# Kernel tuning notes

Measured on AMD Instinct MI355X. Metric: run time of the kernel, lower is better.

The kernel has to match this reference:

```python
import jax, jax.numpy as jnp
import numpy as np

N_NODES = 50000
N_EDGES = 800000
HIDDEN = 256
N_LAYERS = 3
N_PAIRS = 4096


def setup_inputs() -> dict:
    key = jax.random.key(0)
    ks = jax.random.split(key, 10)
    s = 1.0 / np.sqrt(HIDDEN)
    x = jax.random.normal(ks[0], (N_NODES, HIDDEN), dtype=jnp.float32)
    f0_w = jax.random.normal(ks[1], (N_LAYERS, HIDDEN, HIDDEN), dtype=jnp.float32) * s
    f0_b = jax.random.normal(ks[2], (N_LAYERS, HIDDEN), dtype=jnp.float32) * s
    f1_w = jax.random.normal(ks[3], (N_LAYERS, HIDDEN, HIDDEN), dtype=jnp.float32) * s
    f1_b = jax.random.normal(ks[4], (N_LAYERS, HIDDEN), dtype=jnp.float32) * s
    conv_w = jax.random.normal(ks[5], (N_LAYERS, HIDDEN, HIDDEN), dtype=jnp.float32) * s
    conv_b = jax.random.normal(ks[6], (N_LAYERS, HIDDEN), dtype=jnp.float32) * s
    edge_src = jax.random.randint(ks[7], (N_EDGES,), 0, N_NODES, dtype=jnp.int64 if jax.config.jax_enable_x64 else jnp.int32)
    edge_dst = jax.random.randint(ks[8], (N_EDGES,), 0, N_NODES, dtype=edge_src.dtype)
    pos = jax.random.randint(ks[9], (N_PAIRS, 2), 0, N_NODES, dtype=edge_src.dtype)
    return {"x": x, "f0_w": f0_w, "f0_b": f0_b, "f1_w": f1_w, "f1_b": f1_b,
            "conv_w": conv_w, "conv_b": conv_b,
            "edge_src": edge_src, "edge_dst": edge_dst, "pos": pos}


def reference(x, f0_w, f0_b, f1_w, f1_b, conv_w, conv_b, edge_src, edge_dst, pos):
    # Faithful translation of FLabelingNet.forward:
    #   for each layer: x0 = f0(x); x0[idx] = f1(x[idx]); x = conv(x0, adj)
    #   return x[pos]
    n = x.shape[0]
    idx = pos.reshape(-1)  # (2M,) labeled node indices
    for i in range(f0_w.shape[0]):
        x0 = x @ f0_w[i] + f0_b[i]                       # (N, F) elementwise linear
        lbl = x[idx] @ f1_w[i] + f1_b[i]                 # (2M, F) transform of labeled rows
        x0 = x0.at[idx].set(lbl)                         # scatter-overwrite selected rows
        h = x0 @ conv_w[i] + conv_b[i]                   # node-wise linear of the conv
        # sparse adjacency message passing: out[v] = sum_{(u,v) in E} h[u]
        x = jax.ops.segment_sum(h[edge_src], edge_dst, num_segments=n)
    return x[pos]  # (M, 2, F)
```

## Files before the change

kernel.cpp:

```cpp
#include <hip/hip_runtime.h>
#include <hip/hip_bf16.h>

#define N_NODES 50000
#define N_EDGES 800000
#define HIDDEN  256
#define N_LAYERS 3
#define N_PAIRS 4096
#define N_LABEL 8192
#define NPAD    50176
#define SCAN_BLOCKS (NPAD / 256)
#define WSZ (HIDDEN * HIDDEN)

#define NROWPAD (N_NODES + 1)
#define SLICE_ELEMS ((size_t)NROWPAD * 32)
#define SEG_CHUNKS ((N_NODES + 63) / 64)

#define G0_PAIRS   3136
#define G0_TOTAL   (G0_PAIRS + 256)

typedef __bf16 bf16x8 __attribute__((ext_vector_type(8)));
typedef __bf16 bf16x4 __attribute__((ext_vector_type(4)));
typedef float  f32x4  __attribute__((ext_vector_type(4)));
typedef float  f32x2  __attribute__((ext_vector_type(2)));

__device__ __forceinline__ void load_lds16(const void* g, void* l) {
    __builtin_amdgcn_global_load_lds(
        (const __attribute__((address_space(1))) void*)g,
        (__attribute__((address_space(3))) void*)l, 16, 0, 0);
}

__device__ __forceinline__ void acc8(const uint4 w, f32x2* a) {
    a[0] += (f32x2){__uint_as_float(w.x << 16), __uint_as_float(w.x & 0xffff0000u)};
    a[1] += (f32x2){__uint_as_float(w.y << 16), __uint_as_float(w.y & 0xffff0000u)};
    a[2] += (f32x2){__uint_as_float(w.z << 16), __uint_as_float(w.z & 0xffff0000u)};
    a[3] += (f32x2){__uint_as_float(w.w << 16), __uint_as_float(w.w & 0xffff0000u)};
}

template <bool DEG_BIAS, bool A_FP32, bool FILL_PLANE>
__global__ __launch_bounds__(256) void mfma_gemm_fused(
    const void* __restrict__ A_in,
    const __bf16* __restrict__ Wt0, const __bf16* __restrict__ Wt1,
    const float* __restrict__ bD0, const float* __restrict__ bD1,
    const float* __restrict__ bC0, const float* __restrict__ bC1,
    __bf16* __restrict__ Cout,
    const int* __restrict__ idx,
    const int* __restrict__ degv,
    const int* __restrict__ flags,
    const int* __restrict__ esrc,
    const int* __restrict__ edst,
    int* __restrict__ cursor,
    int* __restrict__ ssorted,
    int M)
{
    int role, bx, by;
    if constexpr (FILL_PLANE) {
        const int id = blockIdx.x;
        if (id < G0_PAIRS) {
            const int sub = ((id >> 4) << 3) | (id & 7);
            if ((id >> 3) & 1) {
                int e = sub * 512 + (int)threadIdx.x;
                #pragma unroll
                for (int r = 0; r < 2; ++r) {
                    if (e < N_EDGES) {
                        const int p = atomicAdd(&cursor[edst[e]], 1);
                        ssorted[p] = esrc[e];
                    }
                    e += 256;
                }
                return;
            }
            role = 0; bx = sub >> 1; by = sub & 1;
            if (bx >= 782) return;
        } else {
            const int lb = id - G0_PAIRS;
            role = 1; bx = lb & 127; by = lb >> 7;
        }
    } else {
        role = blockIdx.z; bx = blockIdx.x; by = blockIdx.y;
        if (role == 1 && bx >= N_LABEL / 64) return;
    }

    const __bf16* A   = (const __bf16*)A_in;
    const float*  A32 = (const float*)A_in;
    const __bf16* Wt  = role ? Wt1 : Wt0;
    const float*  bD  = role ? bD1 : bD0;
    const float*  bC  = role ? bC1 : bC0;

    __shared__ __bf16 As[64 * 32];
    __shared__ __bf16 Bs[128 * 32];
    __shared__ int s_idx[64];

    const int t    = threadIdx.x;
    const int lane = t & 63;
    const int wave = t >> 6;
    const int m0   = bx * 64;
    const int n0   = by * 128;

    if (role == 1) {
        if (t < 64) s_idx[t] = idx[m0 + t];
        __syncthreads();
    }

    const int arow  = t >> 2;
    const int acol8 = (t & 3) * 8;
    int anode;
    if (role == 1) {
        anode = s_idx[arow];
    } else {
        const int rg = m0 + arow;
        anode = (rg < M) ? rg : (M - 1);
    }
    const __bf16* aptr   = A   + (size_t)anode * HIDDEN + acol8;
    const float*  aptr32 = A32 + (size_t)anode * HIDDEN + acol8;

    const __bf16* bptr[2];
    #pragma unroll
    for (int r = 0; r < 2; ++r) {
        const int c = r * 256 + t;
        bptr[r] = Wt + (size_t)(n0 + (c >> 2)) * HIDDEN + (c & 3) * 8;
    }

    f32x4 acc[8];
    #pragma unroll
    for (int i = 0; i < 8; ++i) acc[i] = (f32x4){0.f, 0.f, 0.f, 0.f};

    const int wm   = wave * 16;
    const int fm   = lane & 15;
    const int quad = lane >> 4;

    for (int k0 = 0; k0 < HIDDEN; k0 += 32) {
        __syncthreads();
        if constexpr (A_FP32) {
            const float* ap = aptr32 + k0;
            const float4 u0 = *(const float4*)(ap);
            const float4 u1 = *(const float4*)(ap + 4);
            bf16x8 w = {(__bf16)u0.x, (__bf16)u0.y, (__bf16)u0.z, (__bf16)u0.w,
                        (__bf16)u1.x, (__bf16)u1.y, (__bf16)u1.z, (__bf16)u1.w};
            *(bf16x8*)(As + (size_t)t * 8) = w;
        } else {
            load_lds16(aptr + k0, (void*)(As + (size_t)t * 8));
        }
        #pragma unroll
        for (int r = 0; r < 2; ++r)
            load_lds16(bptr[r] + k0, (void*)(Bs + (size_t)(r * 256 + t) * 8));
        __syncthreads();

        const bf16x8 af = *(const bf16x8*)(As + (wm + fm) * 32 + quad * 8);
        bf16x8 bfr[8];
        #pragma unroll
        for (int nt = 0; nt < 8; ++nt)
            bfr[nt] = *(const bf16x8*)(Bs + (nt * 16 + fm) * 32 + quad * 8);

        #pragma unroll
        for (int nt = 0; nt < 8; ++nt)
            acc[nt] = __builtin_amdgcn_mfma_f32_16x16x32_bf16(
                af, bfr[nt], acc[nt], 0, 0, 0);
    }

    float bd[8], bc[8];
    #pragma unroll
    for (int nt = 0; nt < 8; ++nt) {
        const int col = n0 + nt * 16 + fm;
        bd[nt] = DEG_BIAS ? bD[col] : 0.f;
        bc[nt] = bC[col];
    }

    #pragma unroll
    for (int rg = 0; rg < 4; ++rg) {
        const int rloc = wm + quad * 4 + rg;
        int orow;
        if (role == 1) {
            orow = s_idx[rloc];
        } else {
            orow = m0 + rloc;
            if (orow >= M) continue;
            if (flags[orow]) continue;
        }
        float bscale = 0.f;
        if constexpr (DEG_BIAS)
            bscale = (float)degv[orow];
        #pragma unroll
        for (int nt = 0; nt < 8; ++nt) {
            const int cb = n0 + nt * 16;
            float v = acc[nt][rg];
            if constexpr (DEG_BIAS) v += bscale * bd[nt];
            v += bc[nt];
            Cout[(size_t)(cb >> 5) * SLICE_ELEMS + (size_t)orow * 32
                 + (cb & 31) + fm] = (__bf16)v;
        }
    }
}

template <bool GATHER_A, bool DEG_BIAS, bool DEG_VIA_IDX, bool OUT_BF16, bool PROD_BATCH>
__global__ __launch_bounds__(256) void mfma_gemm(
    const __bf16* __restrict__ A_in,
    const __bf16* __restrict__ Wt_in,
    const float* __restrict__ biasD,
    void* __restrict__ Cout_in,
    const int* __restrict__ idx,
    const int* __restrict__ degv,
    int M)
{
    const __bf16* A  = A_in;
    const __bf16* Wt = Wt_in;
    void* Cout = Cout_in;
    if constexpr (PROD_BATCH) {
        const int z = blockIdx.z;
        A    = A_in  + (size_t)(3 * (1 + (z >> 1)) + (z & 1)) * WSZ;
        Wt   = Wt_in + (size_t)(z >> 1) * WSZ;
        Cout = (void*)((__bf16*)Cout_in + (size_t)z * WSZ);
    }

    __shared__ __bf16 As[64 * 32];
    __shared__ __bf16 Bs[128 * 32];
    __shared__ int s_idx[64];

    const int t    = threadIdx.x;
    const int lane = t & 63;
    const int wave = t >> 6;
    const int m0   = blockIdx.x * 64;
    const int n0   = blockIdx.y * 128;

    if constexpr (GATHER_A || DEG_VIA_IDX) {
        if (t < 64) s_idx[t] = idx[m0 + t];
        __syncthreads();
    }

    const int arow  = t >> 2;
    const int acol8 = (t & 3) * 8;
    int anode;
    if constexpr (GATHER_A) {
        anode = s_idx[arow];
    } else {
        const int rg = m0 + arow;
        anode = (rg < M) ? rg : (M - 1);
    }
    const __bf16* aptr = A + (size_t)anode * HIDDEN + acol8;

    const __bf16* bptr[2];
    #pragma unroll
    for (int r = 0; r < 2; ++r) {
        const int c = r * 256 + t;
        bptr[r] = Wt + (size_t)(n0 + (c >> 2)) * HIDDEN + (c & 3) * 8;
    }

    f32x4 acc[8];
    #pragma unroll
    for (int i = 0; i < 8; ++i) acc[i] = (f32x4){0.f, 0.f, 0.f, 0.f};

    const int wm   = wave * 16;
    const int fm   = lane & 15;
    const int quad = lane >> 4;

    for (int k0 = 0; k0 < HIDDEN; k0 += 32) {
        __syncthreads();
        load_lds16(aptr + k0, (void*)(As + (size_t)t * 8));
        #pragma unroll
        for (int r = 0; r < 2; ++r)
            load_lds16(bptr[r] + k0, (void*)(Bs + (size_t)(r * 256 + t) * 8));
        __syncthreads();

        const bf16x8 af = *(const bf16x8*)(As + (wm + fm) * 32 + quad * 8);
        bf16x8 bfr[8];
        #pragma unroll
        for (int nt = 0; nt < 8; ++nt)
            bfr[nt] = *(const bf16x8*)(Bs + (nt * 16 + fm) * 32 + quad * 8);

        #pragma unroll
        for (int nt = 0; nt < 8; ++nt)
            acc[nt] = __builtin_amdgcn_mfma_f32_16x16x32_bf16(
                af, bfr[nt], acc[nt], 0, 0, 0);
    }

    float bd[8];
    #pragma unroll
    for (int nt = 0; nt < 8; ++nt)
        bd[nt] = DEG_BIAS ? biasD[n0 + nt * 16 + fm] : 0.f;

    #pragma unroll
    for (int rg = 0; rg < 4; ++rg) {
        const int rloc = wm + quad * 4 + rg;
        const int orow = m0 + rloc;
        if (!PROD_BATCH && orow >= M) continue;
        int dnode = orow;
        if constexpr (GATHER_A || DEG_VIA_IDX) dnode = s_idx[rloc];
        float bscale = 0.f;
        if constexpr (DEG_BIAS)
            bscale = (float)degv[dnode];
        #pragma unroll
        for (int nt = 0; nt < 8; ++nt) {
            const int col = n0 + nt * 16 + fm;
            float v = acc[nt][rg];
            if constexpr (DEG_BIAS) v += bscale * bd[nt];
            if constexpr (OUT_BF16)
                ((__bf16*)Cout)[(size_t)orow * HIDDEN + col] = (__bf16)v;
            else
                ((float*)Cout)[(size_t)orow * HIDDEN + col] = v;
        }
    }
}

__global__ __launch_bounds__(256) void wconv_kernel(
    const float* __restrict__ f0_w, const float* __restrict__ f1_w,
    const float* __restrict__ conv_w, const float* __restrict__ conv_b,
    __bf16* __restrict__ wt_all, __bf16* __restrict__ cw_nt,
    float* __restrict__ q,
    const int* __restrict__ edge_dst, const int* __restrict__ pos,
    int* __restrict__ counts, int* __restrict__ flags,
    __bf16* __restrict__ x0b)
{
    const int z = blockIdx.z;
    const int tx = threadIdx.x, ty = threadIdx.y;

    if (z >= 12) {
        const int plane = z - 12;
        const int t = ty * 32 + tx;
        const int eb = plane * 64 + blockIdx.x * 8 + blockIdx.y;
        const int e = eb * 256 + t;
        if (e < N_EDGES) atomicAdd(&counts[edge_dst[e]], 1);
        if (e < N_LABEL) flags[pos[e]] = 1;
        if (plane == 0 && blockIdx.x == 0 && blockIdx.y == 0) {
            const int sl = t >> 5, c = t & 31;
            x0b[(size_t)sl * SLICE_ELEMS + (size_t)N_NODES * 32 + c] = (__bf16)0.f;
        }
        return;
    }

    const int kx = blockIdx.x * 32, nx = blockIdx.y * 32;

    if (z < 9) {
        const int layer = z / 3, which = z % 3;
        const float* W = ((which == 0) ? f0_w : (which == 1) ? f1_w : conv_w)
                         + (size_t)layer * WSZ;
        __bf16* T = wt_all + (size_t)z * WSZ;

        __shared__ float tile[32][33];
        for (int i = ty; i < 32; i += 8)
            tile[i][tx] = W[(size_t)(kx + i) * HIDDEN + nx + tx];
        __syncthreads();
        for (int i = ty; i < 32; i += 8)
            T[(size_t)(nx + i) * HIDDEN + kx + tx] = (__bf16)tile[tx][i];
    } else if (z < 11) {
        const int layer = z - 9;
        const float* W = conv_w + (size_t)layer * WSZ;
        __bf16* T = cw_nt + (size_t)layer * WSZ;
        for (int i = ty; i < 32; i += 8)
            T[(size_t)(kx + i) * HIDDEN + nx + tx] =
                (__bf16)W[(size_t)(kx + i) * HIDDEN + nx + tx];
    } else {
        if (blockIdx.x >= 4 || blockIdx.y != 0) return;
        const int zq = blockIdx.x;
        const int l = zq >> 1, branch = zq & 1;
        const float* cb = conv_b + (size_t)l * HIDDEN;
        const float* W  = (branch ? f1_w : f0_w) + (size_t)(l + 1) * WSZ;
        const int n = ty * 32 + tx;
        float s = 0.f;
        #pragma unroll 4
        for (int k = 0; k < HIDDEN; ++k)
            s += cb[k] * W[(size_t)k * HIDDEN + n];
        q[(size_t)zq * HIDDEN + n] = s;
    }
}

__device__ __forceinline__ int block_incl_scan(int v, int* s, int t)
{
    s[t] = v; __syncthreads();
    #pragma unroll
    for (int off = 1; off < 256; off <<= 1) {
        int add = (t >= off) ? s[t - off] : 0;
        __syncthreads();
        s[t] += add;
        __syncthreads();
    }
    return s[t];
}

__global__ __launch_bounds__(256) void scan1_kernel(
    const int* __restrict__ counts, int* __restrict__ offs, int* __restrict__ bsum)
{
    __shared__ int s[256];
    const int t = threadIdx.x;
    const int i = blockIdx.x * 256 + t;
    const int pv = (counts[i] + 7) & ~7;
    int incl = block_incl_scan(pv, s, t);
    offs[i] = incl - pv;
    if (t == 255) bsum[blockIdx.x] = incl;
}

__global__ __launch_bounds__(256) void scan2_kernel(
    const int* __restrict__ bsum, int* __restrict__ bbase)
{
    __shared__ int s[256];
    const int t = threadIdx.x;
    const int v = (t < SCAN_BLOCKS) ? bsum[t] : 0;
    int incl = block_incl_scan(v, s, t);
    bbase[t] = incl - v;
}

__global__ __launch_bounds__(256) void scan3_kernel(
    int* __restrict__ offs, const int* __restrict__ bbase,
    int* __restrict__ cursor, const int* __restrict__ counts,
    int* __restrict__ src_sorted)
{
    const int i = blockIdx.x * 256 + threadIdx.x;
    const int o = offs[i] + bbase[blockIdx.x];
    offs[i] = o;
    cursor[i] = o;
    const int v  = counts[i];
    const int pv = (v + 7) & ~7;
    for (int j = o + v; j < o + pv; ++j) src_sorted[j] = N_NODES;
}

template <bool COMPACT>
__global__ __launch_bounds__(256) void seg_slice_kernel(
    const __bf16* __restrict__ x0b,
    const int* __restrict__ srcs,
    const int* __restrict__ offs,
    const int* __restrict__ nodelist,
    __bf16* __restrict__ out)
{
    const int slice = blockIdx.x & 7;
    const int chunk = blockIdx.x >> 3;
    const int t    = threadIdx.x;
    const int wave = t >> 6;
    const int lane = t & 63;
    const int g    = lane >> 2;
    const int li   = lane & 3;
    const int rw   = chunk * 64 + wave * 16 + g;
    if (!COMPACT && rw >= N_NODES) return;

    const int d    = COMPACT ? nodelist[rw] : rw;
    const int beg  = offs[d];
    const int pdeg = offs[d + 1] - beg;

    const char* xb = (const char*)(x0b + (size_t)slice * SLICE_ELEMS);
    const uint32_t lioff = (uint32_t)li * 16u;
    const int* sp = srcs + beg;

    f32x2 a[4];
    #pragma unroll
    for (int j = 0; j < 4; ++j) a[j] = (f32x2){0.f, 0.f};

    int4 j0, j1;
    if (pdeg > 0) {
        j0 = *(const int4*)(sp);
        j1 = *(const int4*)(sp + 4);
    }

    for (int base = 0; base < pdeg; base += 8) {
        const int4 k0 = j0, k1 = j1;
        if (base + 8 < pdeg) {
            j0 = *(const int4*)(sp + base + 8);
            j1 = *(const int4*)(sp + base + 12);
        }
        const uint4 c0 = *(const uint4*)(xb + (((uint32_t)k0.x << 6) + lioff));
        const uint4 c1 = *(const uint4*)(xb + (((uint32_t)k0.y << 6) + lioff));
        const uint4 c2 = *(const uint4*)(xb + (((uint32_t)k0.z << 6) + lioff));
        const uint4 c3 = *(const uint4*)(xb + (((uint32_t)k0.w << 6) + lioff));
        const uint4 c4 = *(const uint4*)(xb + (((uint32_t)k1.x << 6) + lioff));
        const uint4 c5 = *(const uint4*)(xb + (((uint32_t)k1.y << 6) + lioff));
        const uint4 c6 = *(const uint4*)(xb + (((uint32_t)k1.z << 6) + lioff));
        const uint4 c7 = *(const uint4*)(xb + (((uint32_t)k1.w << 6) + lioff));
        acc8(c0, a); acc8(c1, a); acc8(c2, a); acc8(c3, a);
        acc8(c4, a); acc8(c5, a); acc8(c6, a); acc8(c7, a);
    }

    bf16x8 o;
    #pragma unroll
    for (int j = 0; j < 4; ++j) {
        o[2 * j]     = (__bf16)a[j].x;
        o[2 * j + 1] = (__bf16)a[j].y;
    }
    *(bf16x8*)(out + (size_t)rw * HIDDEN + (slice << 5) + li * 8) = o;
}

extern "C" void kernel_launch(void* const* d_in, const int* in_sizes, int n_in,
                              void* d_out, int out_size, void* d_ws, size_t ws_size,
                              hipStream_t stream)
{
    const float* x       = (const float*)d_in[0];
    const float* f0_w    = (const float*)d_in[1];
    const float* f0_b    = (const float*)d_in[2];
    const float* f1_w    = (const float*)d_in[3];
    const float* f1_b    = (const float*)d_in[4];
    const float* conv_w  = (const float*)d_in[5];
    const float* conv_b  = (const float*)d_in[6];
    const int*   edge_src = (const int*)d_in[7];
    const int*   edge_dst = (const int*)d_in[8];
    const int*   pos      = (const int*)d_in[9];
    float* out = (float*)d_out;

    const size_t buf = (size_t)N_NODES * HIDDEN;

    char* p = (char*)d_ws;
    __bf16* bufA   = (__bf16*)p; p += buf * 2;
    __bf16* bufB   = (__bf16*)p; p += SLICE_ELEMS * 8 * 2;
    __bf16* s_lbl  = (__bf16*)p; p += (size_t)N_LABEL * HIDDEN * 2;
    __bf16* wt_all = (__bf16*)p; p += (size_t)9 * WSZ * 2;
    __bf16* prod   = (__bf16*)p; p += (size_t)4 * WSZ * 2;
    __bf16* cw_nt  = (__bf16*)p; p += (size_t)2 * WSZ * 2;
    float*  qv     = (float*)p;  p += (size_t)4 * HIDDEN * 4;
    int* counts     = (int*)p;  p += NPAD * 4;
    int* flags      = (int*)p;  p += NPAD * 4;
    int* offs       = (int*)p;  p += NPAD * 4;
    int* cursor     = (int*)p;  p += NPAD * 4;
    int* bsum       = (int*)p;  p += 256 * 4;
    int* bbase      = (int*)p;  p += 256 * 4;
    int* src_sorted = (int*)p;  p += (size_t)(N_EDGES + 7 * NPAD) * 4;

    hipMemsetAsync(counts, 0, 2 * NPAD * sizeof(int), stream);
    wconv_kernel<<<dim3(8, 8, 61), dim3(32, 8), 0, stream>>>(
        f0_w, f1_w, conv_w, conv_b, wt_all, cw_nt, qv,
        edge_dst, pos, counts, flags, bufB);
    scan1_kernel<<<SCAN_BLOCKS, 256, 0, stream>>>(counts, offs, bsum);
    scan2_kernel<<<1, 256, 0, stream>>>(bsum, bbase);
    scan3_kernel<<<SCAN_BLOCKS, 256, 0, stream>>>(offs, bbase, cursor, counts, src_sorted);

    mfma_gemm<false, false, false, true, true><<<dim3(4, 2, 4), 256, 0, stream>>>(
        wt_all, cw_nt, nullptr, prod, nullptr, nullptr, HIDDEN);

    const dim3 fused_grid(782, 2, 2);
    const dim3 lbl_grid(128, 2);

    __bf16* cur = bufA;
    __bf16* tmp = bufB;

    for (int l = 0; l < N_LAYERS; ++l) {
        const float* B0 = f0_b + (size_t)l * HIDDEN;
        const float* B1 = f1_b + (size_t)l * HIDDEN;

        if (l == 0) {
            mfma_gemm_fused<false, true, true><<<G0_TOTAL, 256, 0, stream>>>(
                x, wt_all + 0 * WSZ, wt_all + 1 * WSZ,
                nullptr, nullptr, B0, B1, tmp, pos, counts, flags,
                edge_src, edge_dst, cursor, src_sorted, N_NODES);
        } else {
            const int z0 = (l - 1) * 2;
            mfma_gemm_fused<true, false, false><<<fused_grid, 256, 0, stream>>>(
                cur, prod + (size_t)z0 * WSZ, prod + (size_t)(z0 + 1) * WSZ,
                qv + (size_t)z0 * HIDDEN, qv + (size_t)(z0 + 1) * HIDDEN,
                B0, B1, tmp, pos, counts, flags,
                nullptr, nullptr, nullptr, nullptr, N_NODES);
        }

        if (l < N_LAYERS - 1) {
            seg_slice_kernel<false><<<8 * SEG_CHUNKS, 256, 0, stream>>>(
                tmp, src_sorted, offs, nullptr, cur);
        } else {
            seg_slice_kernel<true><<<8 * (N_LABEL / 64), 256, 0, stream>>>(
                tmp, src_sorted, offs, pos, s_lbl);
            mfma_gemm<false, true, true, false, false><<<lbl_grid, 256, 0, stream>>>(
                s_lbl, wt_all + (size_t)(2 * 3 + 2) * WSZ,
                conv_b + (size_t)2 * HIDDEN, out, pos, counts, N_LABEL);
        }
    }
}
```

Baseline: 384.3 us.

## Triple-buffer GEMM K-loop, precast x to bf16, and rank-based edge placement

Both MFMA GEMM kernels now run a 3-stage LDS ring buffer with asynchronous global-to-LDS loads issued two steps ahead. Each step waits with explicit vmcnt and uses one barrier instead of two, so load latency overlaps the MFMA work. The fp32 input x is converted to bf16 in extra blocks of the prep kernel, which lets layer 0 use the async LDS path. The edge bucketing records each edge's atomic rank during counting and places it at offs+rank, replacing a second atomic pass over cursors. The cost is triple the LDS footprint (which may reduce occupancy), an extra N_EDGES rank buffer, and a full extra pass writing x as bf16.

New measurement: 355.2 us. 1.08x faster.

```diff
diff --git a/kernel.cpp b/kernel.cpp
--- a/kernel.cpp
+++ b/kernel.cpp
@@ -10,6 +10,7 @@
 #define NPAD    50176
 #define SCAN_BLOCKS (NPAD / 256)
 #define WSZ (HIDDEN * HIDDEN)
+#define NSTEP (HIDDEN / 32)
 
 #define NROWPAD (N_NODES + 1)
 #define SLICE_ELEMS ((size_t)NROWPAD * 32)
@@ -19,7 +20,6 @@
 #define G0_TOTAL   (G0_PAIRS + 256)
 
 typedef __bf16 bf16x8 __attribute__((ext_vector_type(8)));
-typedef __bf16 bf16x4 __attribute__((ext_vector_type(4)));
 typedef float  f32x4  __attribute__((ext_vector_type(4)));
 typedef float  f32x2  __attribute__((ext_vector_type(2)));
 
@@ -36,9 +36,16 @@
     a[3] += (f32x2){__uint_as_float(w.w << 16), __uint_as_float(w.w & 0xffff0000u)};
 }
 
-template <bool DEG_BIAS, bool A_FP32, bool FILL_PLANE>
+#define GEMM_PIPELINE(APTR, BPTR, AS, BS)                                     \
+    {                                                                          \
+        load_lds16((APTR), (void*)((AS) + (size_t)t * 8));                     \
+        load_lds16((BPTR)[0], (void*)((BS) + (size_t)t * 8));                  \
+        load_lds16((BPTR)[1], (void*)((BS) + (size_t)(256 + t) * 8));          \
+    }
+
+template <bool DEG_BIAS, bool FILL_PLANE>
 __global__ __launch_bounds__(256) void mfma_gemm_fused(
-    const void* __restrict__ A_in,
+    const __bf16* __restrict__ A,
     const __bf16* __restrict__ Wt0, const __bf16* __restrict__ Wt1,
     const float* __restrict__ bD0, const float* __restrict__ bD1,
     const float* __restrict__ bC0, const float* __restrict__ bC1,
@@ -48,7 +55,8 @@
     const int* __restrict__ flags,
     const int* __restrict__ esrc,
     const int* __restrict__ edst,
-    int* __restrict__ cursor,
+    const int* __restrict__ coffs,
+    const int* __restrict__ rankv,
     int* __restrict__ ssorted,
     int M)
 {
@@ -62,8 +70,8 @@
                 #pragma unroll
                 for (int r = 0; r < 2; ++r) {
                     if (e < N_EDGES) {
-                        const int p = atomicAdd(&cursor[edst[e]], 1);
-                        ssorted[p] = esrc[e];
+                        const int d = edst[e];
+                        ssorted[coffs[d] + rankv[e]] = esrc[e];
                     }
                     e += 256;
                 }
@@ -80,14 +88,12 @@
         if (role == 1 && bx >= N_LABEL / 64) return;
     }
 
-    const __bf16* A   = (const __bf16*)A_in;
-    const float*  A32 = (const float*)A_in;
-    const __bf16* Wt  = role ? Wt1 : Wt0;
-    const float*  bD  = role ? bD1 : bD0;
-    const float*  bC  = role ? bC1 : bC0;
-
-    __shared__ __bf16 As[64 * 32];
-    __shared__ __bf16 Bs[128 * 32];
+    const __bf16* Wt = role ? Wt1 : Wt0;
+    const float*  bD = role ? bD1 : bD0;
+    const float*  bC = role ? bC1 : bC0;
+
+    __shared__ __bf16 As[3 * 64 * 32];
+    __shared__ __bf16 Bs[3 * 128 * 32];
     __shared__ int s_idx[64];
 
     const int t    = threadIdx.x;
@@ -110,8 +116,7 @@
         const int rg = m0 + arow;
         anode = (rg < M) ? rg : (M - 1);
     }
-    const __bf16* aptr   = A   + (size_t)anode * HIDDEN + acol8;
-    const float*  aptr32 = A32 + (size_t)anode * HIDDEN + acol8;
+    const __bf16* aptr = A + (size_t)anode * HIDDEN + acol8;
 
     const __bf16* bptr[2];
     #pragma unroll
@@ -128,34 +133,41 @@
     const int fm   = lane & 15;
     const int quad = lane >> 4;
 
-    for (int k0 = 0; k0 < HIDDEN; k0 += 32) {
-        __syncthreads();
-        if constexpr (A_FP32) {
-            const float* ap = aptr32 + k0;
-            const float4 u0 = *(const float4*)(ap);
-            const float4 u1 = *(const float4*)(ap + 4);
-            bf16x8 w = {(__bf16)u0.x, (__bf16)u0.y, (__bf16)u0.z, (__bf16)u0.w,
-                        (__bf16)u1.x, (__bf16)u1.y, (__bf16)u1.z, (__bf16)u1.w};
-            *(bf16x8*)(As + (size_t)t * 8) = w;
-        } else {
-            load_lds16(aptr + k0, (void*)(As + (size_t)t * 8));
-        }
-        #pragma unroll
-        for (int r = 0; r < 2; ++r)
-            load_lds16(bptr[r] + k0, (void*)(Bs + (size_t)(r * 256 + t) * 8));
-        __syncthreads();
-
-        const bf16x8 af = *(const bf16x8*)(As + (wm + fm) * 32 + quad * 8);
+    const __bf16* bp0 = bptr[0];
+    const __bf16* bp1 = bptr[1];
+    #define STAGE_F(SB, K0)                                                    \
+        { load_lds16(aptr + (K0), (void*)(As + (SB) * 2048 + (size_t)t * 8));  \
+          load_lds16(bp0 + (K0),  (void*)(Bs + (SB) * 4096 + (size_t)t * 8));  \
+          load_lds16(bp1 + (K0),  (void*)(Bs + (SB) * 4096 + (size_t)(256 + t) * 8)); }
+
+    STAGE_F(0, 0)
+    STAGE_F(1, 32)
+    asm volatile("s_waitcnt vmcnt(3)" ::: "memory");
+    __builtin_amdgcn_sched_barrier(0);
+    __builtin_amdgcn_s_barrier();
+
+    #pragma unroll
+    for (int step = 0; step < NSTEP; ++step) {
+        const int cur = step % 3;
+        if (step + 2 < NSTEP) {
+            const int nb = (step + 2) % 3;
+            STAGE_F(nb, (step + 2) * 32)
+        }
+        const bf16x8 af = *(const bf16x8*)(As + cur * 2048 + (wm + fm) * 32 + quad * 8);
         bf16x8 bfr[8];
         #pragma unroll
         for (int nt = 0; nt < 8; ++nt)
-            bfr[nt] = *(const bf16x8*)(Bs + (nt * 16 + fm) * 32 + quad * 8);
-
+            bfr[nt] = *(const bf16x8*)(Bs + cur * 4096 + (nt * 16 + fm) * 32 + quad * 8);
         #pragma unroll
         for (int nt = 0; nt < 8; ++nt)
             acc[nt] = __builtin_amdgcn_mfma_f32_16x16x32_bf16(
                 af, bfr[nt], acc[nt], 0, 0, 0);
-    }
+        if (step + 2 < NSTEP) asm volatile("s_waitcnt vmcnt(3)" ::: "memory");
+        else                  asm volatile("s_waitcnt vmcnt(0)" ::: "memory");
+        __builtin_amdgcn_sched_barrier(0);
+        __builtin_amdgcn_s_barrier();
+    }
+    #undef STAGE_F
 
     float bd[8], bc[8];
     #pragma unroll
@@ -211,8 +223,8 @@
         Cout = (void*)((__bf16*)Cout_in + (size_t)z * WSZ);
     }
 
-    __shared__ __bf16 As[64 * 32];
-    __shared__ __bf16 Bs[128 * 32];
+    __shared__ __bf16 As[3 * 64 * 32];
+    __shared__ __bf16 Bs[3 * 128 * 32];
     __shared__ int s_idx[64];
 
     const int t    = threadIdx.x;
@@ -252,25 +264,41 @@
     const int fm   = lane & 15;
     const int quad = lane >> 4;
 
-    for (int k0 = 0; k0 < HIDDEN; k0 += 32) {
-        __syncthreads();
-        load_lds16(aptr + k0, (void*)(As + (size_t)t * 8));
-        #pragma unroll
-        for (int r = 0; r < 2; ++r)
-            load_lds16(bptr[r] + k0, (void*)(Bs + (size_t)(r * 256 + t) * 8));
-        __syncthreads();
-
-        const bf16x8 af = *(const bf16x8*)(As + (wm + fm) * 32 + quad * 8);
+    const __bf16* bp0 = bptr[0];
+    const __bf16* bp1 = bptr[1];
+    #define STAGE_P(SB, K0)                                                    \
+        { load_lds16(aptr + (K0), (void*)(As + (SB) * 2048 + (size_t)t * 8));  \
+          load_lds16(bp0 + (K0),  (void*)(Bs + (SB) * 4096 + (size_t)t * 8));  \
+          load_lds16(bp1 + (K0),  (void*)(Bs + (SB) * 4096 + (size_t)(256 + t) * 8)); }
+
+    STAGE_P(0, 0)
+    STAGE_P(1, 32)
+    asm volatile("s_waitcnt vmcnt(3)" ::: "memory");
+    __builtin_amdgcn_sched_barrier(0);
+    __builtin_amdgcn_s_barrier();
+
+    #pragma unroll
+    for (int step = 0; step < NSTEP; ++step) {
+        const int cur = step % 3;
+        if (step + 2 < NSTEP) {
+            const int nb = (step + 2) % 3;
+            STAGE_P(nb, (step + 2) * 32)
+        }
+        const bf16x8 af = *(const bf16x8*)(As + cur * 2048 + (wm + fm) * 32 + quad * 8);
         bf16x8 bfr[8];
         #pragma unroll
         for (int nt = 0; nt < 8; ++nt)
-            bfr[nt] = *(const bf16x8*)(Bs + (nt * 16 + fm) * 32 + quad * 8);
-
+            bfr[nt] = *(const bf16x8*)(Bs + cur * 4096 + (nt * 16 + fm) * 32 + quad * 8);
         #pragma unroll
         for (int nt = 0; nt < 8; ++nt)
             acc[nt] = __builtin_amdgcn_mfma_f32_16x16x32_bf16(
                 af, bfr[nt], acc[nt], 0, 0, 0);
-    }
+        if (step + 2 < NSTEP) asm volatile("s_waitcnt vmcnt(3)" ::: "memory");
+        else                  asm volatile("s_waitcnt vmcnt(0)" ::: "memory");
+        __builtin_amdgcn_sched_barrier(0);
+        __builtin_amdgcn_s_barrier();
+    }
+    #undef STAGE_P
 
     float bd[8];
     #pragma unroll
@@ -307,20 +335,34 @@
     float* __restrict__ q,
     const int* __restrict__ edge_dst, const int* __restrict__ pos,
     int* __restrict__ counts, int* __restrict__ flags,
-    __bf16* __restrict__ x0b)
+    int* __restrict__ rankv,
+    __bf16* __restrict__ x0b,
+    const float* __restrict__ x32, __bf16* __restrict__ xb16)
 {
     const int z = blockIdx.z;
     const int tx = threadIdx.x, ty = threadIdx.y;
-
+    const int tt = ty * 32 + tx;
+
+    if (z >= 61) {
+        const int c = (z - 61) * 64 + blockIdx.x * 8 + blockIdx.y;
+        const size_t base = ((size_t)c * 256 + tt) * 8;
+        if (base < (size_t)N_NODES * HIDDEN) {
+            const float4 u0 = *(const float4*)(x32 + base);
+            const float4 u1 = *(const float4*)(x32 + base + 4);
+            bf16x8 w = {(__bf16)u0.x, (__bf16)u0.y, (__bf16)u0.z, (__bf16)u0.w,
+                        (__bf16)u1.x, (__bf16)u1.y, (__bf16)u1.z, (__bf16)u1.w};
+            *(bf16x8*)(xb16 + base) = w;
+        }
+        return;
+    }
     if (z >= 12) {
         const int plane = z - 12;
-        const int t = ty * 32 + tx;
         const int eb = plane * 64 + blockIdx.x * 8 + blockIdx.y;
-        const int e = eb * 256 + t;
-        if (e < N_EDGES) atomicAdd(&counts[edge_dst[e]], 1);
+        const int e = eb * 256 + tt;
+        if (e < N_EDGES) rankv[e] = atomicAdd(&counts[edge_dst[e]], 1);
         if (e < N_LABEL) flags[pos[e]] = 1;
         if (plane == 0 && blockIdx.x == 0 && blockIdx.y == 0) {
-            const int sl = t >> 5, c = t & 31;
+            const int sl = tt >> 5, c = tt & 31;
             x0b[(size_t)sl * SLICE_ELEMS + (size_t)N_NODES * 32 + c] = (__bf16)0.f;
         }
         return;
@@ -353,7 +395,7 @@
         const int l = zq >> 1, branch = zq & 1;
         const float* cb = conv_b + (size_t)l * HIDDEN;
         const float* W  = (branch ? f1_w : f0_w) + (size_t)(l + 1) * WSZ;
-        const int n = ty * 32 + tx;
+        const int n = tt;
         float s = 0.f;
         #pragma unroll 4
         for (int k = 0; k < HIDDEN; ++k)
@@ -399,13 +441,11 @@
 
 __global__ __launch_bounds__(256) void scan3_kernel(
     int* __restrict__ offs, const int* __restrict__ bbase,
-    int* __restrict__ cursor, const int* __restrict__ counts,
-    int* __restrict__ src_sorted)
+    const int* __restrict__ counts, int* __restrict__ src_sorted)
 {
     const int i = blockIdx.x * 256 + threadIdx.x;
     const int o = offs[i] + bbase[blockIdx.x];
     offs[i] = o;
-    cursor[i] = o;
     const int v  = counts[i];
     const int pv = (v + 7) & ~7;
     for (int j = o + v; j < o + pv; ++j) src_sorted[j] = N_NODES;
@@ -503,18 +543,18 @@
     int* counts     = (int*)p;  p += NPAD * 4;
     int* flags      = (int*)p;  p += NPAD * 4;
     int* offs       = (int*)p;  p += NPAD * 4;
-    int* cursor     = (int*)p;  p += NPAD * 4;
     int* bsum       = (int*)p;  p += 256 * 4;
     int* bbase      = (int*)p;  p += 256 * 4;
+    int* rankv      = (int*)p;  p += (size_t)N_EDGES * 4;
     int* src_sorted = (int*)p;  p += (size_t)(N_EDGES + 7 * NPAD) * 4;
 
     hipMemsetAsync(counts, 0, 2 * NPAD * sizeof(int), stream);
-    wconv_kernel<<<dim3(8, 8, 61), dim3(32, 8), 0, stream>>>(
+    wconv_kernel<<<dim3(8, 8, 159), dim3(32, 8), 0, stream>>>(
         f0_w, f1_w, conv_w, conv_b, wt_all, cw_nt, qv,
-        edge_dst, pos, counts, flags, bufB);
+        edge_dst, pos, counts, flags, rankv, bufB, x, bufA);
     scan1_kernel<<<SCAN_BLOCKS, 256, 0, stream>>>(counts, offs, bsum);
     scan2_kernel<<<1, 256, 0, stream>>>(bsum, bbase);
-    scan3_kernel<<<SCAN_BLOCKS, 256, 0, stream>>>(offs, bbase, cursor, counts, src_sorted);
+    scan3_kernel<<<SCAN_BLOCKS, 256, 0, stream>>>(offs, bbase, counts, src_sorted);
 
     mfma_gemm<false, false, false, true, true><<<dim3(4, 2, 4), 256, 0, stream>>>(
         wt_all, cw_nt, nullptr, prod, nullptr, nullptr, HIDDEN);
@@ -530,17 +570,17 @@
         const float* B1 = f1_b + (size_t)l * HIDDEN;
 
         if (l == 0) {
-            mfma_gemm_fused<false, true, true><<<G0_TOTAL, 256, 0, stream>>>(
-                x, wt_all + 0 * WSZ, wt_all + 1 * WSZ,
+            mfma_gemm_fused<false, true><<<G0_TOTAL, 256, 0, stream>>>(
+                bufA, wt_all + 0 * WSZ, wt_all + 1 * WSZ,
                 nullptr, nullptr, B0, B1, tmp, pos, counts, flags,
-                edge_src, edge_dst, cursor, src_sorted, N_NODES);
+                edge_src, edge_dst, offs, rankv, src_sorted, N_NODES);
         } else {
             const int z0 = (l - 1) * 2;
-            mfma_gemm_fused<true, false, false><<<fused_grid, 256, 0, stream>>>(
+            mfma_gemm_fused<true, false><<<fused_grid, 256, 0, stream>>>(
                 cur, prod + (size_t)z0 * WSZ, prod + (size_t)(z0 + 1) * WSZ,
                 qv + (size_t)z0 * HIDDEN, qv + (size_t)(z0 + 1) * HIDDEN,
                 B0, B1, tmp, pos, counts, flags,
-                nullptr, nullptr, nullptr, nullptr, N_NODES);
+                nullptr, nullptr, nullptr, nullptr, nullptr, N_NODES);
         }
 
         if (l < N_LAYERS - 1) {
```
